# Optimization experiments

Measured on AMD Instinct MI355X. Metric: run time of the kernel, lower is better.

The kernel has to match this reference:

```python
import jax, jax.numpy as jnp
import numpy as np

B, S, D, H, ADJ = 32, 512, 512, 8, 512
HD = D // H  # 64
NEG_SLOPE = 0.2


def layer_norm(x, g, b, eps=1e-5):
    m = jnp.mean(x, axis=-1, keepdims=True)
    v = jnp.var(x, axis=-1, keepdims=True)
    return (x - m) / jnp.sqrt(v + eps) * g + b


def setup_inputs() -> dict:
    key = jax.random.key(0)
    ks = jax.random.split(key, 8)
    def n(k, shape, s=0.02):
        return jax.random.normal(k, shape, dtype=jnp.float32) * s
    return {
        'x': jax.random.normal(ks[0], (B, S, D), dtype=jnp.float32),
        'adj': jax.random.normal(ks[1], (B, S, ADJ), dtype=jnp.float32),
        'w_W': n(ks[2], (D, D)), 'w_b': jnp.zeros((D,), jnp.float32),
        'a_w': n(ks[3], (2 * HD,)),
        'sem_W': n(ks[4], (D, ADJ)), 'sem_b': jnp.zeros((D,), jnp.float32),
        'ff1_W': n(ks[5], (2 * D, D)), 'ff1_b': jnp.zeros((2 * D,), jnp.float32),
        'ff2_W': n(ks[6], (D, 2 * D)), 'ff2_b': jnp.zeros((D,), jnp.float32),
        'ln1_g': jnp.ones((D,), jnp.float32), 'ln1_b': jnp.zeros((D,), jnp.float32),
        'ln2_g': jnp.ones((D,), jnp.float32), 'ln2_b': jnp.zeros((D,), jnp.float32),
    }


def reference(x, adj, w_W, w_b, a_w, sem_W, sem_b, ff1_W, ff1_b, ff2_W, ff2_b,
              ln1_g, ln1_b, ln2_g, ln2_b):
    residual = x
    # semantic adjacency: Linear(adj_dim -> out_dim) then softmax; out_dim == S
    adj_s = jax.nn.softmax(adj @ sem_W.T + sem_b, axis=-1)  # (B, S, S)

    # GATConv: projection + additive attention.
    # a([h_i, h_j]) == a_src . h_i + a_dst . h_j  (linear, no bias), so the
    # O(S^2 * 2*hd) concat of the original is replaced by a broadcast-add
    # of two per-node scores — identical math.
    h = (x @ w_W.T + w_b).reshape(B, S, H, HD).transpose(0, 2, 1, 3)  # (B,H,S,hd)
    a_src, a_dst = a_w[:HD], a_w[HD:]
    src = jnp.einsum('bhsd,d->bhs', h, a_src)  # score contribution of node i
    dst = jnp.einsum('bhsd,d->bhs', h, a_dst)  # score contribution of node j
    e = jax.nn.leaky_relu(src[:, :, :, None] + dst[:, :, None, :], NEG_SLOPE)
    e = jnp.where(adj_s[:, None, :, :] == 0, -1e9, e)  # masked_fill(adj==0)
    attn = jax.nn.softmax(e, axis=-1)  # (B, H, S, S)
    out = jnp.einsum('bhij,bhjd->bhid', attn, h)  # weighted aggregate
    out = out.transpose(0, 2, 1, 3).reshape(B, S, D)

    out = layer_norm(out + residual, ln1_g, ln1_b)
    residual2 = out
    ff = jax.nn.gelu(out @ ff1_W.T + ff1_b, approximate=False) @ ff2_W.T + ff2_b
    return layer_norm(ff + residual2, ln2_g, ln2_b)
```

## Files before the change

kernel.cpp:

```cpp
#include <hip/hip_runtime.h>
#include <cstdint>
#include <cstddef>


typedef __bf16 bfx8 __attribute__((ext_vector_type(8)));
typedef float v4f __attribute__((ext_vector_type(4)));
typedef unsigned short u16x8 __attribute__((ext_vector_type(8)));

__device__ __forceinline__ float bf2f(unsigned short h) {
    unsigned int u = ((unsigned int)h) << 16;
    return __builtin_bit_cast(float, u);
}
__device__ __forceinline__ unsigned short f2bf(float x) {
    unsigned int u = __builtin_bit_cast(unsigned int, x);
    unsigned int r = (u + 0x7fffu + ((u >> 16) & 1u)) >> 16;
    return (unsigned short)r;
}
__device__ __forceinline__ u16x8 load8cvt(const float* p) {
    float4 a = *(const float4*)p;
    float4 b = *(const float4*)(p + 4);
    u16x8 r;
    r[0] = f2bf(a.x); r[1] = f2bf(a.y); r[2] = f2bf(a.z); r[3] = f2bf(a.w);
    r[4] = f2bf(b.x); r[5] = f2bf(b.y); r[6] = f2bf(b.z); r[7] = f2bf(b.w);
    return r;
}
__device__ __forceinline__ void gl_lds16(const unsigned short* g, unsigned short* l) {
    __builtin_amdgcn_global_load_lds((const __attribute__((address_space(1))) void*)g,
                                     (__attribute__((address_space(3))) void*)l, 16, 0, 0);
}

__global__ __launch_bounds__(256) void cvt_kernel(const float* __restrict__ in,
                                                  unsigned short* __restrict__ out) {
    const int id = blockIdx.x * 256 + threadIdx.x;
    *(u16x8*)(out + (size_t)id * 8) = load8cvt(in + (size_t)id * 8);
}

#define BM 128
#define BN 128
#define BK 32

template <int EPI, typename CT>
__global__ __launch_bounds__(256, 2) void gemm_bt(
    const unsigned short* __restrict__ A, const float* __restrict__ Bw,
    const float* __restrict__ bias, CT* __restrict__ C,
    int M, int N, int K) {
    __shared__ unsigned short sA[BM * BK];
    __shared__ unsigned short sB[BN * BK];
    const int t = threadIdx.x;
    const int lane = t & 63;
    const int w = t >> 6;
    const int wm = w >> 1, wn = w & 1;
    const int m0 = blockIdx.x * BM, n0 = blockIdx.y * BN;
    const int mrow = lane & 15, kq = lane >> 4;

    v4f acc[4][4];
#pragma unroll
    for (int i = 0; i < 4; i++)
#pragma unroll
        for (int j = 0; j < 4; j++) acc[i][j] = (v4f)(0.0f);

    const int r0 = t >> 2;
    const int c0 = (t & 3) * 8;
    const unsigned short* pA0 = A + (size_t)(m0 + r0) * K + c0;
    const unsigned short* pA1 = A + (size_t)(m0 + 64 + r0) * K + c0;
    const float* pB0 = Bw + (size_t)(n0 + r0) * K + c0;
    const float* pB1 = Bw + (size_t)(n0 + 64 + r0) * K + c0;

    for (int k0 = 0; k0 < K; k0 += BK) {
        gl_lds16(pA0 + k0, &sA[t * 8]);
        gl_lds16(pA1 + k0, &sA[(t + 256) * 8]);
        u16x8 b0 = load8cvt(pB0 + k0);
        u16x8 b1 = load8cvt(pB1 + k0);
        *(u16x8*)&sB[t * 8] = b0;
        *(u16x8*)&sB[(t + 256) * 8] = b1;
        __syncthreads();
        bfx8 af[4], bfr[4];
#pragma unroll
        for (int mi = 0; mi < 4; mi++)
            af[mi] = __builtin_bit_cast(bfx8, *(const u16x8*)&sA[(wm * 64 + mi * 16 + mrow) * BK + kq * 8]);
#pragma unroll
        for (int ni = 0; ni < 4; ni++)
            bfr[ni] = __builtin_bit_cast(bfx8, *(const u16x8*)&sB[(wn * 64 + ni * 16 + mrow) * BK + kq * 8]);
#pragma unroll
        for (int mi = 0; mi < 4; mi++)
#pragma unroll
            for (int ni = 0; ni < 4; ni++)
                acc[mi][ni] = __builtin_amdgcn_mfma_f32_16x16x32_bf16(af[mi], bfr[ni], acc[mi][ni], 0, 0, 0);
        __syncthreads();
    }
#pragma unroll
    for (int ni = 0; ni < 4; ni++) {
        const int col = n0 + wn * 64 + ni * 16 + mrow;
        const float bv = bias[col];
#pragma unroll
        for (int mi = 0; mi < 4; mi++) {
#pragma unroll
            for (int r = 0; r < 4; r++) {
                const int row = m0 + wm * 64 + mi * 16 + kq * 4 + r;
                float val = acc[mi][ni][r] + bv;
                if (EPI == 1) val = 0.5f * val * (1.0f + erff(val * 0.70710678118654752f));
                if constexpr (__is_same(CT, float)) C[(size_t)row * N + col] = val;
                else C[(size_t)row * N + col] = f2bf(val);
            }
        }
    }
}

__global__ __launch_bounds__(256) void srcdst_kernel(
    const unsigned short* __restrict__ hbuf, const float* __restrict__ aw,
    float* __restrict__ src, float* __restrict__ dst) {
    const int id = blockIdx.x * 256 + threadIdx.x;
    const int i = id & 511;
    const int bh = id >> 9;
    const int head = bh & 7, b = bh >> 3;
    const unsigned short* hp = hbuf + ((size_t)(b * 512 + i)) * 512 + head * 64;
    float s = 0.f, d = 0.f;
#pragma unroll
    for (int c = 0; c < 8; c++) {
        u16x8 hv = *(const u16x8*)(hp + c * 8);
        float4 a0 = *(const float4*)(aw + c * 8);
        float4 a1 = *(const float4*)(aw + c * 8 + 4);
        float4 d0 = *(const float4*)(aw + 64 + c * 8);
        float4 d1 = *(const float4*)(aw + 64 + c * 8 + 4);
        float av[8] = {a0.x, a0.y, a0.z, a0.w, a1.x, a1.y, a1.z, a1.w};
        float dv[8] = {d0.x, d0.y, d0.z, d0.w, d1.x, d1.y, d1.z, d1.w};
#pragma unroll
        for (int j = 0; j < 8; j++) {
            float x = bf2f(hv[j]);
            s += x * av[j];
            d += x * dv[j];
        }
    }
    src[id] = s;
    dst[id] = d;
}

__global__ __launch_bounds__(256, 2) void attn_kernel(
    const unsigned short* __restrict__ hbuf, const float* __restrict__ srcg,
    const float* __restrict__ dstg, unsigned short* __restrict__ aout) {
    __shared__ unsigned short Ht[64 * 512];

    const int t = threadIdx.x, lane = t & 63, w = t >> 6;
    const int bh = blockIdx.x, b = bh >> 3, head = bh & 7;
    const size_t hbase = (size_t)(b * 512) * 512 + head * 64;

    {
        const int d = lane;
        const int sw = d & 7;
#pragma unroll
        for (int jc = 0; jc < 16; ++jc) {
            const int j0 = w * 128 + jc * 8;
            u16x8 pack;
#pragma unroll
            for (int jj = 0; jj < 8; jj++)
                pack[jj] = hbuf[hbase + (size_t)(j0 + jj) * 512 + d];
            const int gj = (j0 >> 3) ^ sw;
            *(u16x8*)&Ht[d * 512 + gj * 8] = pack;
        }
    }
    __syncthreads();

    float dmax = -1e30f;
#pragma unroll
    for (int q = 0; q < 8; q++) dmax = fmaxf(dmax, dstg[bh * 512 + q * 64 + lane]);
#pragma unroll
    for (int off = 32; off >= 1; off >>= 1) dmax = fmaxf(dmax, __shfl_xor(dmax, off, 64));

    const int mrow = lane & 15, kq = lane >> 4;

#pragma unroll 1
    for (int g = 0; g < 8; ++g) {
        const int ibase = w * 128 + g * 16;
        const float si = srcg[bh * 512 + ibase + mrow];
        const float e0 = si + dmax;
        const float mi = e0 > 0.f ? e0 : 0.2f * e0;
        float sum = 0.f;
        v4f acc[4];
#pragma unroll
        for (int nt = 0; nt < 4; nt++) acc[nt] = (v4f)(0.0f);

#pragma unroll 2
        for (int ks = 0; ks < 16; ++ks) {
            const int j0 = ks * 32 + kq * 8;
            float4 d0 = *(const float4*)&dstg[bh * 512 + j0];
            float4 d1 = *(const float4*)&dstg[bh * 512 + j0 + 4];
            float dj[8] = {d0.x, d0.y, d0.z, d0.w, d1.x, d1.y, d1.z, d1.w};
            u16x8 au;
#pragma unroll
            for (int jj = 0; jj < 8; jj++) {
                float e = si + dj[jj];
                e = e > 0.f ? e : 0.2f * e;
                float p = __expf(e - mi);
                sum += p;
                au[jj] = f2bf(p);
            }
            bfx8 af = __builtin_bit_cast(bfx8, au);
#pragma unroll
            for (int nt = 0; nt < 4; nt++) {
                const int dd = nt * 16 + mrow;
                const int gj = (ks * 4 + kq) ^ (dd & 7);
                bfx8 bfrag = __builtin_bit_cast(bfx8, *(const u16x8*)&Ht[dd * 512 + gj * 8]);
                acc[nt] = __builtin_amdgcn_mfma_f32_16x16x32_bf16(af, bfrag, acc[nt], 0, 0, 0);
            }
        }
        sum += __shfl_xor(sum, 16, 64);
        sum += __shfl_xor(sum, 32, 64);
#pragma unroll
        for (int r = 0; r < 4; r++) {
            const float rs = __shfl(sum, kq * 4 + r, 64);
            const float inv = 1.0f / rs;
            const int row = b * 512 + ibase + kq * 4 + r;
#pragma unroll
            for (int nt = 0; nt < 4; nt++) {
                const int col = head * 64 + nt * 16 + mrow;
                aout[(size_t)row * 512 + col] = f2bf(acc[nt][r] * inv);
            }
        }
    }
}

template <typename T>
__device__ __forceinline__ void loadf8(const T* p, float* v) {
    if constexpr (__is_same(T, float)) {
        float4 a = *(const float4*)p;
        float4 b = *(const float4*)(p + 4);
        v[0] = a.x; v[1] = a.y; v[2] = a.z; v[3] = a.w;
        v[4] = b.x; v[5] = b.y; v[6] = b.z; v[7] = b.w;
    } else {
        u16x8 h = *(const u16x8*)p;
#pragma unroll
        for (int j = 0; j < 8; j++) v[j] = bf2f(h[j]);
    }
}

template <typename XT, typename RT, typename OT>
__global__ __launch_bounds__(256) void ln_kernel(
    const XT* __restrict__ xin, const RT* __restrict__ res,
    const float* __restrict__ gg, const float* __restrict__ bb,
    OT* __restrict__ out) {
    const int row = blockIdx.x * 4 + (threadIdx.x >> 6);
    const int lane = threadIdx.x & 63;
    const size_t base = (size_t)row * 512 + lane * 8;
    float xv[8], rv[8], v[8];
    loadf8(xin + base, xv);
    loadf8(res + base, rv);
    float s1 = 0.f, s2 = 0.f;
#pragma unroll
    for (int j = 0; j < 8; j++) {
        v[j] = xv[j] + rv[j];
        s1 += v[j];
        s2 += v[j] * v[j];
    }
#pragma unroll
    for (int off = 1; off < 64; off <<= 1) {
        s1 += __shfl_xor(s1, off, 64);
        s2 += __shfl_xor(s2, off, 64);
    }
    const float mean = s1 * (1.0f / 512.0f);
    const float var = s2 * (1.0f / 512.0f) - mean * mean;
    const float rstd = rsqrtf(var + 1e-5f);
    float gv[8], bv[8];
    loadf8(gg + lane * 8, gv);
    loadf8(bb + lane * 8, bv);
    float o[8];
#pragma unroll
    for (int j = 0; j < 8; j++) o[j] = (v[j] - mean) * rstd * gv[j] + bv[j];
    if constexpr (__is_same(OT, float)) {
        *(float4*)(out + base) = make_float4(o[0], o[1], o[2], o[3]);
        *(float4*)(out + base + 4) = make_float4(o[4], o[5], o[6], o[7]);
    } else {
        u16x8 ov;
#pragma unroll
        for (int j = 0; j < 8; j++) ov[j] = f2bf(o[j]);
        *(u16x8*)(out + base) = ov;
    }
}

extern "C" void kernel_launch(void* const* d_in, const int* in_sizes, int n_in,
                              void* d_out, int out_size, void* d_ws, size_t ws_size,
                              hipStream_t stream) {
    const float* x   = (const float*)d_in[0];
    const float* wW  = (const float*)d_in[2];
    const float* wb  = (const float*)d_in[3];
    const float* aw  = (const float*)d_in[4];
    const float* f1W = (const float*)d_in[7];
    const float* f1b = (const float*)d_in[8];
    const float* f2W = (const float*)d_in[9];
    const float* f2b = (const float*)d_in[10];
    const float* g1  = (const float*)d_in[11];
    const float* b1  = (const float*)d_in[12];
    const float* g2  = (const float*)d_in[13];
    const float* b2  = (const float*)d_in[14];
    float* out = (float*)d_out;

    char* ws = (char*)d_ws;
    unsigned short* xb    = (unsigned short*)(ws);
    unsigned short* hb    = (unsigned short*)(ws + 16777216);
    unsigned short* aoutb = (unsigned short*)(ws);
    float* src            = (float*)(ws + 33554432);
    float* dst            = (float*)(ws + 33554432 + 524288);
    unsigned short* gbuf  = (unsigned short*)(ws + 16777216);
    unsigned short* y     = (unsigned short*)(ws);

    (void)in_sizes; (void)n_in; (void)out_size; (void)ws_size;

    dim3 blk(256);
    cvt_kernel<<<dim3(4096), blk, 0, stream>>>(x, xb);
    gemm_bt<0, unsigned short><<<dim3(128, 4), blk, 0, stream>>>(xb, wW, wb, hb, 16384, 512, 512);
    srcdst_kernel<<<dim3(512), blk, 0, stream>>>(hb, aw, src, dst);
    attn_kernel<<<dim3(256), blk, 0, stream>>>(hb, src, dst, aoutb);
    ln_kernel<unsigned short, float, unsigned short>
        <<<dim3(4096), blk, 0, stream>>>(aoutb, x, g1, b1, y);
    gemm_bt<1, unsigned short><<<dim3(128, 8), blk, 0, stream>>>(y, f1W, f1b, gbuf, 16384, 1024, 512);
    gemm_bt<0, float><<<dim3(128, 4), blk, 0, stream>>>(gbuf, f2W, f2b, out, 16384, 512, 1024);
    ln_kernel<float, unsigned short, float>
        <<<dim3(4096), blk, 0, stream>>>(out, y, g2, b2, out);
}
```

Measured before the change: 296.3 us.

## Pre-convert GEMM weights to bf16, use async LDS loads for B, swizzle LDS

Adds cvt kernels that convert the three weight matrices to bf16 in workspace once per call. Both GEMM operands can then be staged with global_load_lds instead of per-tile fp32 loads and conversion in registers. The K tile doubles to 64, and LDS uses an XOR-swizzled chunk layout to avoid bank conflicts on fragment reads. The occupancy hint rises to 4 blocks per CU. The cost is three extra small kernel launches, twice the LDS per block, and moving the src/dst buffers to a new workspace offset.

```diff
diff --git a/kernel.cpp b/kernel.cpp
--- a/kernel.cpp
+++ b/kernel.cpp
@@ -37,11 +37,11 @@
 
 #define BM 128
 #define BN 128
-#define BK 32
+#define BK 64
 
 template <int EPI, typename CT>
-__global__ __launch_bounds__(256, 2) void gemm_bt(
-    const unsigned short* __restrict__ A, const float* __restrict__ Bw,
+__global__ __launch_bounds__(256, 4) void gemm_bt(
+    const unsigned short* __restrict__ A, const unsigned short* __restrict__ Bw,
     const float* __restrict__ bias, CT* __restrict__ C,
     int M, int N, int K) {
     __shared__ unsigned short sA[BM * BK];
@@ -59,33 +59,44 @@
 #pragma unroll
         for (int j = 0; j < 4; j++) acc[i][j] = (v4f)(0.0f);
 
-    const int r0 = t >> 2;
-    const int c0 = (t & 3) * 8;
-    const unsigned short* pA0 = A + (size_t)(m0 + r0) * K + c0;
-    const unsigned short* pA1 = A + (size_t)(m0 + 64 + r0) * K + c0;
-    const float* pB0 = Bw + (size_t)(n0 + r0) * K + c0;
-    const float* pB1 = Bw + (size_t)(n0 + 64 + r0) * K + c0;
+    const int sr = t >> 3;
+    const int sc = ((t & 7) ^ (sr & 7)) * 8;
+    const unsigned short* pA[4];
+    const unsigned short* pB[4];
+#pragma unroll
+    for (int c = 0; c < 4; c++) {
+        pA[c] = A + (size_t)(m0 + c * 32 + sr) * K + sc;
+        pB[c] = Bw + (size_t)(n0 + c * 32 + sr) * K + sc;
+    }
 
     for (int k0 = 0; k0 < K; k0 += BK) {
-        gl_lds16(pA0 + k0, &sA[t * 8]);
-        gl_lds16(pA1 + k0, &sA[(t + 256) * 8]);
-        u16x8 b0 = load8cvt(pB0 + k0);
-        u16x8 b1 = load8cvt(pB1 + k0);
-        *(u16x8*)&sB[t * 8] = b0;
-        *(u16x8*)&sB[(t + 256) * 8] = b1;
+#pragma unroll
+        for (int c = 0; c < 4; c++) {
+            gl_lds16(pA[c] + k0, &sA[(c * 256 + t) * 8]);
+            gl_lds16(pB[c] + k0, &sB[(c * 256 + t) * 8]);
+        }
         __syncthreads();
-        bfx8 af[4], bfr[4];
-#pragma unroll
-        for (int mi = 0; mi < 4; mi++)
-            af[mi] = __builtin_bit_cast(bfx8, *(const u16x8*)&sA[(wm * 64 + mi * 16 + mrow) * BK + kq * 8]);
-#pragma unroll
-        for (int ni = 0; ni < 4; ni++)
-            bfr[ni] = __builtin_bit_cast(bfx8, *(const u16x8*)&sB[(wn * 64 + ni * 16 + mrow) * BK + kq * 8]);
-#pragma unroll
-        for (int mi = 0; mi < 4; mi++)
-#pragma unroll
-            for (int ni = 0; ni < 4; ni++)
-                acc[mi][ni] = __builtin_amdgcn_mfma_f32_16x16x32_bf16(af[mi], bfr[ni], acc[mi][ni], 0, 0, 0);
+#pragma unroll
+        for (int kh = 0; kh < 2; kh++) {
+            bfx8 af[4], bfr[4];
+#pragma unroll
+            for (int mi = 0; mi < 4; mi++) {
+                const int r = wm * 64 + mi * 16 + mrow;
+                const int ch = (kh * 4 + kq) ^ (mrow & 7);
+                af[mi] = __builtin_bit_cast(bfx8, *(const u16x8*)&sA[r * BK + ch * 8]);
+            }
+#pragma unroll
+            for (int ni = 0; ni < 4; ni++) {
+                const int r = wn * 64 + ni * 16 + mrow;
+                const int ch = (kh * 4 + kq) ^ (mrow & 7);
+                bfr[ni] = __builtin_bit_cast(bfx8, *(const u16x8*)&sB[r * BK + ch * 8]);
+            }
+#pragma unroll
+            for (int mi = 0; mi < 4; mi++)
+#pragma unroll
+                for (int ni = 0; ni < 4; ni++)
+                    acc[mi][ni] = __builtin_amdgcn_mfma_f32_16x16x32_bf16(af[mi], bfr[ni], acc[mi][ni], 0, 0, 0);
+        }
         __syncthreads();
     }
 #pragma unroll
@@ -297,22 +308,28 @@
     unsigned short* xb    = (unsigned short*)(ws);
     unsigned short* hb    = (unsigned short*)(ws + 16777216);
     unsigned short* aoutb = (unsigned short*)(ws);
-    float* src            = (float*)(ws + 33554432);
-    float* dst            = (float*)(ws + 33554432 + 524288);
     unsigned short* gbuf  = (unsigned short*)(ws + 16777216);
     unsigned short* y     = (unsigned short*)(ws);
+    float* src            = (float*)(ws + 50331648);
+    float* dst            = (float*)(ws + 50331648 + 524288);
+    unsigned short* wWb   = (unsigned short*)(ws + 52428800);
+    unsigned short* f1Wb  = (unsigned short*)(ws + 53477376);
+    unsigned short* f2Wb  = (unsigned short*)(ws + 55574528);
 
     (void)in_sizes; (void)n_in; (void)out_size; (void)ws_size;
 
     dim3 blk(256);
     cvt_kernel<<<dim3(4096), blk, 0, stream>>>(x, xb);
-    gemm_bt<0, unsigned short><<<dim3(128, 4), blk, 0, stream>>>(xb, wW, wb, hb, 16384, 512, 512);
+    cvt_kernel<<<dim3(128), blk, 0, stream>>>(wW, wWb);
+    cvt_kernel<<<dim3(256), blk, 0, stream>>>(f1W, f1Wb);
+    cvt_kernel<<<dim3(256), blk, 0, stream>>>(f2W, f2Wb);
+    gemm_bt<0, unsigned short><<<dim3(128, 4), blk, 0, stream>>>(xb, wWb, wb, hb, 16384, 512, 512);
     srcdst_kernel<<<dim3(512), blk, 0, stream>>>(hb, aw, src, dst);
     attn_kernel<<<dim3(256), blk, 0, stream>>>(hb, src, dst, aoutb);
     ln_kernel<unsigned short, float, unsigned short>
         <<<dim3(4096), blk, 0, stream>>>(aoutb, x, g1, b1, y);
-    gemm_bt<1, unsigned short><<<dim3(128, 8), blk, 0, stream>>>(y, f1W, f1b, gbuf, 16384, 1024, 512);
-    gemm_bt<0, float><<<dim3(128, 4), blk, 0, stream>>>(gbuf, f2W, f2b, out, 16384, 512, 1024);
+    gemm_bt<1, unsigned short><<<dim3(128, 8), blk, 0, stream>>>(y, f1Wb, f1b, gbuf, 16384, 1024, 512);
+    gemm_bt<0, float><<<dim3(128, 4), blk, 0, stream>>>(gbuf, f2Wb, f2b, out, 16384, 512, 1024);
     ln_kernel<float, unsigned short, float>
         <<<dim3(4096), blk, 0, stream>>>(out, y, g2, b2, out);
 }
```

Result: faster. 277.4 us (-6.4%).
